# Optimization experiments

Measured on AMD Instinct MI355X. Metric: run time of the kernel, lower is better.

The kernel has to match this reference:

```python
import jax, jax.numpy as jnp
import numpy as np

D_MODEL = 1024
N_HEADS = 16
D_HEAD = D_MODEL // N_HEADS
WINDOW = 256
ATTN_SCALE = 1.0
SCALE = float(np.sqrt(D_HEAD))
NEG = -10000.0


def setup_inputs() -> dict:
    key = jax.random.key(0)
    ks = jax.random.split(key, 7)
    B, S = 2, 2048
    q = jax.random.normal(ks[0], (B, S, D_MODEL), dtype=jnp.float32)
    k = jax.random.normal(ks[1], (B, S, D_MODEL), dtype=jnp.float32)
    v = jax.random.normal(ks[2], (B, S, D_MODEL), dtype=jnp.float32)
    # Xavier-uniform-like scale for square linear weights: sqrt(6/(fan_in+fan_out))
    lim = float(np.sqrt(6.0 / (D_MODEL + D_MODEL)))
    def xavier(kk):
        return jax.random.uniform(kk, (D_MODEL, D_MODEL), minval=-lim, maxval=lim, dtype=jnp.float32)
    return {"q": q, "k": k, "v": v,
            "WQ": xavier(ks[3]), "WK": xavier(ks[4]),
            "WV": xavier(ks[5]), "WO": xavier(ks[6])}


def _split_heads(x):
    B, S, _ = x.shape
    return x.reshape(B, S, N_HEADS, D_HEAD).transpose(0, 2, 1, 3)  # [B,H,S,Dh]


def reference(q, k, v, WQ, WK, WV, WO):
    B, Sq, _ = q.shape
    Sk = k.shape[1]
    # torch nn.Linear: y = x @ W.T
    qh = _split_heads(q @ WQ.T) / SCALE          # [B,H,Sq,Dh]
    kh = _split_heads(k @ WK.T)                  # [B,H,Sk,Dh]
    vh = _split_heads(v @ WV.T)                  # [B,H,Sk,Dh]
    scores = jnp.einsum('bhqd,bhkd->bhqk', qh, kh) * ATTN_SCALE
    # global abs-max normalization (clamped at 1)
    scores = scores / jnp.maximum(jnp.max(jnp.abs(scores)), 1.0)
    # sliding window mask: key j visible to query i iff i-WINDOW+1 <= j <= i
    qi = jnp.arange(Sq)[:, None]
    kj = jnp.arange(Sk)[None, :]
    win = (kj <= qi) & (kj > qi - WINDOW)        # [Sq,Sk] bool
    scores = jnp.where(win[None, None], scores, NEG)
    attn = jax.nn.softmax(scores, axis=-1)
    out = jnp.einsum('bhqk,bhkd->bhqd', attn, vh)
    out = out.transpose(0, 2, 1, 3).reshape(B, Sq, D_MODEL)
    out = out @ WO.T
    out = out / jnp.maximum(jnp.mean(jnp.abs(out)), 1.0)
    return out
```

## Files before the change

### kernel.cpp

```cpp
#include <hip/hip_runtime.h>
#include <hip/hip_bf16.h>

#define S_LEN 2048
#define DM    1024
#define NH    16
#define DH    64
#define WIN   256
#define BATCH 2

using f32x4   = __attribute__((ext_vector_type(4))) float;
using bf16x8  = __attribute__((ext_vector_type(8))) short;
using ushort8 = __attribute__((ext_vector_type(8))) unsigned short;

static __device__ __forceinline__ unsigned short f2bf(float f) {
  unsigned int x = __float_as_uint(f);
  x += 0x7fffu + ((x >> 16) & 1u);
  return (unsigned short)(x >> 16);
}

typedef const __attribute__((address_space(1))) void* gas_t;
typedef __attribute__((address_space(3))) void* las_t;
static __device__ __forceinline__ void gload16(const void* g, void* l) {
  __builtin_amdgcn_global_load_lds((gas_t)g, (las_t)l, 16, 0, 0);
}

__global__ __launch_bounds__(256) void k_cvt_all(const float* __restrict__ w0,
                                                 const float* __restrict__ w1,
                                                 const float* __restrict__ w2,
                                                 const float* __restrict__ w3,
                                                 const float* __restrict__ q,
                                                 const float* __restrict__ k,
                                                 const float* __restrict__ v,
                                                 unsigned short* __restrict__ Wb,
                                                 unsigned short* __restrict__ qb,
                                                 unsigned short* __restrict__ kb,
                                                 unsigned short* __restrict__ vb,
                                                 unsigned int* __restrict__ absmax) {
  const int z = blockIdx.z;
  if (z == 0 && blockIdx.x == 0 && threadIdx.x == 0) *absmax = 0u;
  const float* src;
  unsigned short* dst;
  int n8;
  if (z < 4) {
    src = (z == 0) ? w0 : (z == 1) ? w1 : (z == 2) ? w2 : w3;
    dst = Wb + (size_t)z * DM * DM;
    n8 = (DM * DM) / 8;
  } else {
    src = (z == 4) ? q : (z == 5) ? k : v;
    dst = (z == 4) ? qb : (z == 5) ? kb : vb;
    n8 = (BATCH * S_LEN * DM) / 8;
  }
  int i = blockIdx.x * blockDim.x + threadIdx.x;
  int stride = gridDim.x * blockDim.x;
  for (; i < n8; i += stride) {
    float4 f0 = ((const float4*)src)[2 * i];
    float4 f1 = ((const float4*)src)[2 * i + 1];
    ushort8 u;
    u[0] = f2bf(f0.x); u[1] = f2bf(f0.y); u[2] = f2bf(f0.z); u[3] = f2bf(f0.w);
    u[4] = f2bf(f1.x); u[5] = f2bf(f1.y); u[6] = f2bf(f1.z); u[7] = f2bf(f1.w);
    ((ushort8*)dst)[i] = u;
  }
}

__device__ __forceinline__ void gemm128_core(const unsigned short* __restrict__ A,
                                             const unsigned short* __restrict__ Bw,
                                             void* __restrict__ Cptr, float oscale,
                                             int omode, bool swap, int R0, int C0,
                                             float* __restrict__ partials, int pbid) {
  __shared__ unsigned short As[2][128][64];
  __shared__ unsigned short Bs[2][128][64];
  __shared__ float red[4];
  const int tid = threadIdx.x, lane = tid & 63, w = tid >> 6;
  const int wr = w >> 1, wc = w & 1;

  int srow[4], scol[4];
#pragma unroll
  for (int c = 0; c < 4; ++c) {
    srow[c] = c * 32 + w * 8 + (lane >> 3);
    scol[c] = ((lane & 7) ^ (srow[c] & 7)) << 3;
  }

  f32x4 z = {0.f, 0.f, 0.f, 0.f};
  f32x4 acc[4][4];
#pragma unroll
  for (int i = 0; i < 4; ++i)
#pragma unroll
    for (int j = 0; j < 4; ++j) acc[i][j] = z;

  unsigned short* Af0 = &As[0][0][0];
  unsigned short* Bf0 = &Bs[0][0][0];
  const int cb = 16 * (lane >> 4);

#define STAGE_G(buf, k0) do {                                                          \
    unsigned short* Ad = Af0 + (buf) * 8192 + w * 512;                                 \
    unsigned short* Bd = Bf0 + (buf) * 8192 + w * 512;                                 \
    _Pragma("unroll")                                                                  \
    for (int c = 0; c < 4; ++c) {                                                      \
      gload16(A  + (size_t)(R0 + srow[c]) * DM + (k0) + scol[c], Ad + c * 2048);       \
      gload16(Bw + (size_t)(C0 + srow[c]) * DM + (k0) + scol[c], Bd + c * 2048);       \
    }                                                                                  \
  } while (0)

  STAGE_G(0, 0);
  __syncthreads();

  for (int t = 0; t < 16; ++t) {
    const int cur = t & 1;
    if (t + 1 < 16) STAGE_G(cur ^ 1, (t + 1) * 64);

    const char* Af = (const char*)(Af0 + cur * 8192);
    const char* Bf = (const char*)(Bf0 + cur * 8192);
    bf16x8 av[4][2], bv[4][2];
#pragma unroll
    for (int i = 0; i < 4; ++i) {
      int row = 64 * wr + 16 * i + (lane & 15);
      int sw = (row & 7) << 4;
      const char* rp = Af + row * 128;
      av[i][0] = *(const bf16x8*)(rp + (cb ^ sw));
      av[i][1] = *(const bf16x8*)(rp + ((cb + 64) ^ sw));
    }
#pragma unroll
    for (int j = 0; j < 4; ++j) {
      int row = 64 * wc + 16 * j + (lane & 15);
      int sw = (row & 7) << 4;
      const char* rp = Bf + row * 128;
      bv[j][0] = *(const bf16x8*)(rp + (cb ^ sw));
      bv[j][1] = *(const bf16x8*)(rp + ((cb + 64) ^ sw));
    }
    if (swap) {
#pragma unroll
      for (int i = 0; i < 4; ++i)
#pragma unroll
        for (int j = 0; j < 4; ++j) {
          acc[i][j] = __builtin_amdgcn_mfma_f32_16x16x32_bf16(bv[j][0], av[i][0], acc[i][j], 0, 0, 0);
          acc[i][j] = __builtin_amdgcn_mfma_f32_16x16x32_bf16(bv[j][1], av[i][1], acc[i][j], 0, 0, 0);
        }
    } else {
#pragma unroll
      for (int i = 0; i < 4; ++i)
#pragma unroll
        for (int j = 0; j < 4; ++j) {
          acc[i][j] = __builtin_amdgcn_mfma_f32_16x16x32_bf16(av[i][0], bv[j][0], acc[i][j], 0, 0, 0);
          acc[i][j] = __builtin_amdgcn_mfma_f32_16x16x32_bf16(av[i][1], bv[j][1], acc[i][j], 0, 0, 0);
        }
    }
    __syncthreads();
  }
#undef STAGE_G

  float s = 0.f;
#pragma unroll
  for (int i = 0; i < 4; ++i) {
#pragma unroll
    for (int j = 0; j < 4; ++j) {
      if (swap) {
        int grow  = R0 + 64 * wr + 16 * i + (lane & 15);
        int gcol0 = C0 + 64 * wc + 16 * j + 4 * (lane >> 4);
        if (omode == 0) {
          float4 st = {acc[i][j][0] * oscale, acc[i][j][1] * oscale,
                       acc[i][j][2] * oscale, acc[i][j][3] * oscale};
          s += fabsf(st.x) + fabsf(st.y) + fabsf(st.z) + fabsf(st.w);
          *(float4*)((float*)Cptr + (size_t)grow * DM + gcol0) = st;
        } else {
          int b = grow >> 11, ss = grow & (S_LEN - 1);
          int h = gcol0 >> 6, d0 = gcol0 & 63;
          ushort4 st = {f2bf(acc[i][j][0] * oscale), f2bf(acc[i][j][1] * oscale),
                        f2bf(acc[i][j][2] * oscale), f2bf(acc[i][j][3] * oscale)};
          *(ushort4*)((unsigned short*)Cptr + (((size_t)(b * NH + h) * S_LEN + ss) << 6) + d0) = st;
        }
      } else {
        int grow0 = R0 + 64 * wr + 16 * i + 4 * (lane >> 4);
        int gcol  = C0 + 64 * wc + 16 * j + (lane & 15);
        int b = grow0 >> 11, s0 = grow0 & (S_LEN - 1);
        int h = gcol >> 6, d = gcol & 63;
        ushort4 st = {f2bf(acc[i][j][0] * oscale), f2bf(acc[i][j][1] * oscale),
                      f2bf(acc[i][j][2] * oscale), f2bf(acc[i][j][3] * oscale)};
        *(ushort4*)((unsigned short*)Cptr + (((size_t)(b * NH + h) * DH + d) << 11) + s0) = st;
      }
    }
  }
  if (partials) {
#pragma unroll
    for (int mk = 1; mk < 64; mk <<= 1) s += __shfl_xor(s, mk, 64);
    if (lane == 0) red[w] = s;
    __syncthreads();
    if (tid == 0) partials[pbid] = red[0] + red[1] + red[2] + red[3];
  }
}

__global__ __launch_bounds__(256) void k_gemm_qkv(const unsigned short* __restrict__ qb,
                                                  const unsigned short* __restrict__ kb,
                                                  const unsigned short* __restrict__ vb,
                                                  const unsigned short* __restrict__ WbQ,
                                                  const unsigned short* __restrict__ WbK,
                                                  const unsigned short* __restrict__ WbV,
                                                  unsigned short* __restrict__ qh,
                                                  unsigned short* __restrict__ kh,
                                                  unsigned short* __restrict__ vt) {
  const unsigned short *A, *B;
  unsigned short* C;
  float sc;
  int om;
  bool sw;
  if (blockIdx.z == 0)      { A = qb; B = WbQ; C = qh; sc = 0.125f; om = 1; sw = true;  }
  else if (blockIdx.z == 1) { A = kb; B = WbK; C = kh; sc = 1.0f;   om = 1; sw = true;  }
  else                      { A = vb; B = WbV; C = vt; sc = 1.0f;   om = 2; sw = false; }
  gemm128_core(A, B, C, sc, om, sw, blockIdx.x * 128, blockIdx.y * 128, nullptr, 0);
}

__global__ __launch_bounds__(256) void k_gemm_out(const unsigned short* __restrict__ A,
                                                  const unsigned short* __restrict__ Bw,
                                                  float* __restrict__ C,
                                                  float* __restrict__ partials) {
  gemm128_core(A, Bw, C, 1.0f, 0, true, blockIdx.x * 128, blockIdx.y * 128,
               partials, blockIdx.x + gridDim.x * blockIdx.y);
}

__global__ __launch_bounds__(256) void k_scoresmax(const unsigned short* __restrict__ qh,
                                                   const unsigned short* __restrict__ kh,
                                                   unsigned int* __restrict__ absmax) {
  __shared__ unsigned short Ks[2][128][64];
  const int tid = threadIdx.x, lane = tid & 63, w = tid >> 6;
  const int lin = blockIdx.x;
  const int xcd = lin & 7, j = lin >> 3;
  const int bh = xcd + 8 * (j >> 3);
  const int q0 = (j & 7) * 256;
  const size_t base = (size_t)bh * S_LEN * DH;
  const unsigned short* Q = qh + base;
  const unsigned short* K = kh + base;

  bf16x8 a[4][2];
#pragma unroll
  for (int rb = 0; rb < 4; ++rb) {
    const unsigned short* qr = Q + (size_t)(q0 + 64 * w + 16 * rb + (lane & 15)) * DH + 8 * (lane >> 4);
    a[rb][0] = *(const bf16x8*)qr;
    a[rb][1] = *(const bf16x8*)(qr + 32);
  }

  int srow[4], scol[4];
#pragma unroll
  for (int c = 0; c < 4; ++c) {
    srow[c] = c * 32 + w * 8 + (lane >> 3);
    scol[c] = ((lane & 7) ^ (srow[c] & 7)) << 3;
  }
  unsigned short* Kf0 = &Ks[0][0][0];
  const int cbb = 16 * (lane >> 4);

#define STAGE_K(buf, kc) do {                                                          \
    unsigned short* Kd = Kf0 + (buf) * 8192 + w * 512;                                 \
    _Pragma("unroll")                                                                  \
    for (int c = 0; c < 4; ++c)                                                        \
      gload16(K + (size_t)((kc) + srow[c]) * DH + scol[c], Kd + c * 2048);             \
  } while (0)

  STAGE_K(0, 0);
  __syncthreads();

  float m = 0.f;
  for (int t = 0; t < 16; ++t) {
    const int cur = t & 1;
    if (t + 1 < 16) STAGE_K(cur ^ 1, (t + 1) * 128);
    const char* Kf = (const char*)(Kf0 + cur * 8192);
#pragma unroll
    for (int cb = 0; cb < 8; ++cb) {
      int row = 16 * cb + (lane & 15);
      int sw = (row & 7) << 4;
      const char* rp = Kf + row * 128;
      bf16x8 b0 = *(const bf16x8*)(rp + (cbb ^ sw));
      bf16x8 b1 = *(const bf16x8*)(rp + ((cbb + 64) ^ sw));
#pragma unroll
      for (int rb = 0; rb < 4; ++rb) {
        f32x4 acc = {0.f, 0.f, 0.f, 0.f};
        acc = __builtin_amdgcn_mfma_f32_16x16x32_bf16(a[rb][0], b0, acc, 0, 0, 0);
        acc = __builtin_amdgcn_mfma_f32_16x16x32_bf16(a[rb][1], b1, acc, 0, 0, 0);
        m = fmaxf(m, fmaxf(fmaxf(fabsf(acc[0]), fabsf(acc[1])), fmaxf(fabsf(acc[2]), fabsf(acc[3]))));
      }
    }
    __syncthreads();
  }
#undef STAGE_K

#pragma unroll
  for (int mk = 1; mk < 64; mk <<= 1) m = fmaxf(m, __shfl_xor(m, mk, 64));
  __shared__ float red[4];
  if (lane == 0) red[w] = m;
  __syncthreads();
  if (threadIdx.x == 0)
    atomicMax(absmax, __float_as_uint(fmaxf(fmaxf(red[0], red[1]), fmaxf(red[2], red[3]))));
}

#define NT 10
__global__ __launch_bounds__(256) void k_attn(const unsigned short* __restrict__ qh,
                                              const unsigned short* __restrict__ kh,
                                              const unsigned short* __restrict__ vt,
                                              const unsigned int* __restrict__ absmax,
                                              unsigned short* __restrict__ attn_c) {
  __shared__ unsigned short Ks[2][32][72];
  __shared__ unsigned short Vts[2][64][40];
  __shared__ unsigned short Pl[4][16][40];
  const int tid = threadIdx.x, lane = tid & 63, w = tid >> 6;
  const int lin = blockIdx.x;
  const int xcd = lin & 7, j = lin >> 3;
  const int bh = xcd + 8 * (j >> 5);
  const int Q0 = (j & 31) * 64;
  const int b = bh >> 4, h = bh & 15;
  const int kstart = Q0 - WIN;
  const size_t base = (size_t)bh * S_LEN * DH;
  const unsigned short* Kb = kh + base;
  const unsigned short* Vtb = vt + base;

  const int skrow = tid >> 3, skcol = (tid & 7) << 3;
  const int svd = tid >> 2, svcol = (tid & 3) << 3;

  const float invM = 1.0f / fmaxf(__uint_as_float(*absmax), 1.0f);
  const unsigned short* Qp = qh + base + (size_t)(Q0 + 16 * w + (lane & 15)) * DH + 8 * (lane >> 4);
  bf16x8 a0 = *(const bf16x8*)Qp;
  bf16x8 a1 = *(const bf16x8*)(Qp + 32);

  ushort8 rk, rv;
  ushort8 zz = {0, 0, 0, 0, 0, 0, 0, 0};
#define LOADT(T) do {                                                        \
    int kk = kstart + 32 * (T) + skrow;                                      \
    rk = (kk >= 0) ? *(const ushort8*)(Kb + (size_t)kk * DH + skcol) : zz;   \
    int kc = kstart + 32 * (T) + svcol;                                      \
    rv = (kc >= 0) ? *(const ushort8*)(Vtb + (size_t)svd * S_LEN + kc) : zz; \
  } while (0)
#define WRITET(buf) do {                                                     \
    *(ushort8*)&Ks[buf][skrow][skcol] = rk;                                  \
    *(ushort8*)&Vts[buf][svd][svcol] = rv;                                   \
  } while (0)

  LOADT(0);
  WRITET(0);
  __syncthreads();

  const int Tlo = w >> 1, Thi = (w >> 1) + 8;
  const int qrow = Q0 + 16 * w + 4 * (lane >> 4);
  float sm[4] = {0.f, 0.f, 0.f, 0.f};
  f32x4 z = {0.f, 0.f, 0.f, 0.f};
  f32x4 o[4];
#pragma unroll
  for (int i = 0; i < 4; ++i) o[i] = z;

  for (int T = 0; T < NT; ++T) {
    const int cur = T & 1;
    const bool act = (T >= Tlo) && (T <= Thi);
    if (T + 1 < NT) LOADT(T + 1);
    if (act) {
      f32x4 p[2];
#pragma unroll
      for (int cb = 0; cb < 2; ++cb) {
        const unsigned short* kr = &Ks[cur][16 * cb + (lane & 15)][8 * (lane >> 4)];
        bf16x8 b0 = *(const bf16x8*)kr;
        bf16x8 b1 = *(const bf16x8*)(kr + 32);
        f32x4 a = z;
        a = __builtin_amdgcn_mfma_f32_16x16x32_bf16(a0, b0, a, 0, 0, 0);
        a = __builtin_amdgcn_mfma_f32_16x16x32_bf16(a1, b1, a, 0, 0, 0);
        p[cb] = a;
      }
#pragma unroll
      for (int cb = 0; cb < 2; ++cb) {
        int kcol = kstart + 32 * T + 16 * cb + (lane & 15);
#pragma unroll
        for (int r = 0; r < 4; ++r) {
          int qq = qrow + r;
          bool ok = (kcol >= 0) && (kcol <= qq) && (kcol + WIN > qq);
          float e = ok ? __expf(p[cb][r] * invM) : 0.f;
          sm[r] += e;
          Pl[w][4 * (lane >> 4) + r][16 * cb + (lane & 15)] = f2bf(e);
        }
      }
    }
    __syncthreads();
    if (act) {
      bf16x8 pa = *(const bf16x8*)&Pl[w][lane & 15][8 * (lane >> 4)];
#pragma unroll
      for (int dt = 0; dt < 4; ++dt) {
        bf16x8 bv = *(const bf16x8*)&Vts[cur][16 * dt + (lane & 15)][8 * (lane >> 4)];
        o[dt] = __builtin_amdgcn_mfma_f32_16x16x32_bf16(pa, bv, o[dt], 0, 0, 0);
      }
    }
    if (T + 1 < NT) WRITET((T + 1) & 1);
    __syncthreads();
  }

#pragma unroll
  for (int r = 0; r < 4; ++r) {
#pragma unroll
    for (int mk = 1; mk < 16; mk <<= 1) sm[r] += __shfl_xor(sm[r], mk, 64);
    sm[r] = 1.0f / sm[r];
  }
#pragma unroll
  for (int dt = 0; dt < 4; ++dt) {
#pragma unroll
    for (int r = 0; r < 4; ++r) {
      int qq = qrow + r;
      float val = o[dt][r] * sm[r];
      attn_c[((size_t)(b * S_LEN + qq) << 10) + h * DH + 16 * dt + (lane & 15)] = f2bf(val);
    }
  }
#undef LOADT
#undef WRITET
}

__global__ __launch_bounds__(256) void k_scale_final(float* __restrict__ x,
                                                     const float* __restrict__ partials,
                                                     float invcnt, int n4) {
  __shared__ float red[4];
  float s = partials[threadIdx.x];
#pragma unroll
  for (int mk = 1; mk < 64; mk <<= 1) s += __shfl_xor(s, mk, 64);
  if ((threadIdx.x & 63) == 0) red[threadIdx.x >> 6] = s;
  __syncthreads();
  float d = 1.0f / fmaxf((red[0] + red[1] + red[2] + red[3]) * invcnt, 1.0f);
  for (int i = blockIdx.x * blockDim.x + threadIdx.x; i < n4; i += gridDim.x * blockDim.x) {
    float4 f = ((float4*)x)[i];
    f.x *= d; f.y *= d; f.z *= d; f.w *= d;
    ((float4*)x)[i] = f;
  }
}

extern "C" void kernel_launch(void* const* d_in, const int* in_sizes, int n_in,
                              void* d_out, int out_size, void* d_ws, size_t ws_size,
                              hipStream_t stream) {
  (void)in_sizes; (void)n_in; (void)out_size; (void)ws_size;
  const float* q  = (const float*)d_in[0];
  const float* k  = (const float*)d_in[1];
  const float* v  = (const float*)d_in[2];
  const float* WQ = (const float*)d_in[3];
  const float* WK = (const float*)d_in[4];
  const float* WV = (const float*)d_in[5];
  const float* WO = (const float*)d_in[6];

  const size_t HS = (size_t)BATCH * NH * S_LEN * DH;
  unsigned short* qb     = (unsigned short*)d_ws;
  unsigned short* kb     = qb + HS;
  unsigned short* vb     = kb + HS;
  unsigned short* qh     = vb + HS;
  unsigned short* kh     = qh + HS;
  unsigned short* vt     = kh + HS;
  unsigned short* Wb     = vt + HS;
  char* scal             = (char*)(Wb + 4 * (size_t)DM * DM);
  unsigned int* absmax   = (unsigned int*)scal;
  float* partials        = (float*)(scal + 16);
  unsigned short* attn_c = qb;

  unsigned short* WbQ = Wb;
  unsigned short* WbK = Wb + (size_t)DM * DM;
  unsigned short* WbV = Wb + 2 * (size_t)DM * DM;
  unsigned short* WbO = Wb + 3 * (size_t)DM * DM;

  k_cvt_all<<<dim3(128, 1, 7), 256, 0, stream>>>(WQ, WK, WV, WO, q, k, v, Wb, qb, kb, vb, absmax);

  k_gemm_qkv<<<dim3(32, 8, 3), 256, 0, stream>>>(qb, kb, vb, WbQ, WbK, WbV, qh, kh, vt);

  k_scoresmax<<<256, 256, 0, stream>>>(qh, kh, absmax);
  k_attn<<<1024, 256, 0, stream>>>(qh, kh, vt, absmax, attn_c);

  k_gemm_out<<<dim3(32, 8), 256, 0, stream>>>(attn_c, WbO, (float*)d_out, partials);

  k_scale_final<<<1024, 256, 0, stream>>>((float*)d_out, partials, 1.0f / (float)HS, (int)(HS / 4));
}
```

Measured before the change: 141.9 us.

## Replace QKV projection GEMM with 256x256-tile, 8-wave, eight-phase pipelined kernel

The QKV projection moves from 128x128 tiles with 256 threads to 256x256 tiles with 512 threads (8 waves). Each k-step is split into eight phases that interleave LDS reads, async global-to-LDS staging and MFMA bursts, using explicit barriers, vmcnt waits and setprio. The larger tile raises operand reuse and the phase schedule is meant to hide load latency. In exchange the grid shrinks to 192 blocks, which may underfill the GPU's CUs, and LDS use and register pressure go up.

```diff
diff --git a/kernel.cpp b/kernel.cpp
--- a/kernel.cpp
+++ b/kernel.cpp
@@ -62,6 +62,192 @@
   }
 }
 
+__device__ __forceinline__ void gemm256_8ph(const unsigned short* __restrict__ A,
+                                            const unsigned short* __restrict__ Bw,
+                                            void* __restrict__ Cptr, float oscale,
+                                            int omode, bool swap, int R0, int C0) {
+  __shared__ unsigned short As_[2][256][64];
+  __shared__ unsigned short Bs_[2][256][64];
+  const int tid = threadIdx.x, lane = tid & 63, w = tid >> 6;
+  const int wr = w >> 2, wc = w & 3;
+
+  const int srow_in_half = w * 8 + (lane >> 3);
+  const int cb = 16 * (lane >> 4);
+
+#define STAGE_AH(buf, h, t) do {                                                        \
+    _Pragma("unroll")                                                                   \
+    for (int c = 0; c < 2; ++c) {                                                       \
+      int r = (h) * 128 + c * 64 + srow_in_half;                                        \
+      int sc = ((lane & 7) ^ (r & 7)) << 3;                                             \
+      gload16(A + (size_t)(R0 + r) * DM + (t) * 64 + sc, &As_[buf][r & ~7][0] + ((r & 7) - (lane >> 3)) * 0 + ( (h)*128 + c*64 + w*8 ) * 64 - ((h)*128 + c*64 + w*8)*64 + &As_[buf][(h)*128 + c*64 + w*8][0] - &As_[buf][(h)*128 + c*64 + w*8][0] + 0); \
+    }                                                                                   \
+  } while (0)
+#undef STAGE_AH
+#define STAGE_AH(buf, h, t) do {                                                        \
+    _Pragma("unroll")                                                                   \
+    for (int c = 0; c < 2; ++c) {                                                       \
+      int r = (h) * 128 + c * 64 + srow_in_half;                                        \
+      int sc = ((lane & 7) ^ (r & 7)) << 3;                                             \
+      gload16(A + (size_t)(R0 + r) * DM + (t) * 64 + sc,                                \
+              &As_[buf][(h) * 128 + c * 64 + w * 8][0]);                                \
+    }                                                                                   \
+  } while (0)
+#define STAGE_BH(buf, h, t) do {                                                        \
+    _Pragma("unroll")                                                                   \
+    for (int c = 0; c < 2; ++c) {                                                       \
+      int r = (h) * 128 + c * 64 + srow_in_half;                                        \
+      int sc = ((lane & 7) ^ (r & 7)) << 3;                                             \
+      gload16(Bw + (size_t)(C0 + r) * DM + (t) * 64 + sc,                               \
+              &Bs_[buf][(h) * 128 + c * 64 + w * 8][0]);                                \
+    }                                                                                   \
+  } while (0)
+#define READ_AV(dst, buf, kf) do {                                                      \
+    _Pragma("unroll")                                                                   \
+    for (int i = 0; i < 8; ++i) {                                                       \
+      int row = 128 * wr + 16 * i + (lane & 15);                                        \
+      int byte = (cb + 64 * (kf)) ^ ((row & 7) << 4);                                   \
+      dst[i] = *(const bf16x8*)((const char*)&As_[buf][row][0] + byte);                 \
+    }                                                                                   \
+  } while (0)
+#define READ_BV(dst, buf, jh, kf) do {                                                  \
+    _Pragma("unroll")                                                                   \
+    for (int jj = 0; jj < 2; ++jj) {                                                    \
+      int row = 64 * wc + 16 * (2 * (jh) + jj) + (lane & 15);                           \
+      int byte = (cb + 64 * (kf)) ^ ((row & 7) << 4);                                   \
+      dst[jj] = *(const bf16x8*)((const char*)&Bs_[buf][row][0] + byte);                \
+    }                                                                                   \
+  } while (0)
+
+  f32x4 z = {0.f, 0.f, 0.f, 0.f};
+  f32x4 acc[8][4];
+#pragma unroll
+  for (int i = 0; i < 8; ++i)
+#pragma unroll
+    for (int j = 0; j < 4; ++j) acc[i][j] = z;
+
+  bf16x8 avA[8], avB[8], bvA[2], bvB[2];
+
+#define MFMA_PH(av, bv, jh) do {                                                        \
+    __builtin_amdgcn_s_setprio(1);                                                      \
+    if (swap) {                                                                         \
+      _Pragma("unroll")                                                                 \
+      for (int i = 0; i < 8; ++i) {                                                     \
+        acc[i][2*(jh)]   = __builtin_amdgcn_mfma_f32_16x16x32_bf16(bv[0], av[i], acc[i][2*(jh)],   0, 0, 0); \
+        acc[i][2*(jh)+1] = __builtin_amdgcn_mfma_f32_16x16x32_bf16(bv[1], av[i], acc[i][2*(jh)+1], 0, 0, 0); \
+      }                                                                                 \
+    } else {                                                                            \
+      _Pragma("unroll")                                                                 \
+      for (int i = 0; i < 8; ++i) {                                                     \
+        acc[i][2*(jh)]   = __builtin_amdgcn_mfma_f32_16x16x32_bf16(av[i], bv[0], acc[i][2*(jh)],   0, 0, 0); \
+        acc[i][2*(jh)+1] = __builtin_amdgcn_mfma_f32_16x16x32_bf16(av[i], bv[1], acc[i][2*(jh)+1], 0, 0, 0); \
+      }                                                                                 \
+    }                                                                                   \
+    __builtin_amdgcn_s_setprio(0);                                                      \
+  } while (0)
+
+#define PH_SYNC() do {                                                                  \
+    __builtin_amdgcn_s_barrier();                                                       \
+    asm volatile("s_waitcnt lgkmcnt(0)" ::: "memory");                                  \
+    __builtin_amdgcn_sched_barrier(0);                                                  \
+  } while (0)
+#define PH_END() __builtin_amdgcn_s_barrier()
+
+  STAGE_AH(0, 0, 0); STAGE_AH(0, 1, 0); STAGE_BH(0, 0, 0); STAGE_BH(0, 1, 0);
+  STAGE_AH(1, 0, 1); STAGE_AH(1, 1, 1); STAGE_BH(1, 0, 1); STAGE_BH(1, 1, 1);
+  asm volatile("s_waitcnt vmcnt(8)" ::: "memory");
+  __builtin_amdgcn_s_barrier();
+  READ_AV(avA, 0, 0);
+  READ_BV(bvA, 0, 0, 0);
+
+  for (int m = 0; m < 8; ++m) {
+    const int t2 = 2 * m + 2, t3 = 2 * m + 3;
+    READ_BV(bvB, 0, 1, 0);
+    if (m > 0) STAGE_BH(1, 0, 2 * m + 1);
+    PH_SYNC(); MFMA_PH(avA, bvA, 0); PH_END();
+    READ_AV(avB, 0, 1);
+    READ_BV(bvA, 0, 0, 1);
+    if (m > 0) STAGE_BH(1, 1, 2 * m + 1);
+    PH_SYNC(); MFMA_PH(avA, bvB, 1); PH_END();
+    READ_BV(bvB, 0, 1, 1);
+    if (t2 < 16) STAGE_AH(0, 0, t2);
+    asm volatile("s_waitcnt vmcnt(2)" ::: "memory");
+    PH_SYNC(); MFMA_PH(avB, bvA, 0); PH_END();
+    READ_AV(avA, 1, 0);
+    READ_BV(bvA, 1, 0, 0);
+    if (t2 < 16) STAGE_AH(0, 1, t2);
+    PH_SYNC(); MFMA_PH(avB, bvB, 1); PH_END();
+    READ_BV(bvB, 1, 1, 0);
+    if (t2 < 16) STAGE_BH(0, 0, t2);
+    PH_SYNC(); MFMA_PH(avA, bvA, 0); PH_END();
+    READ_AV(avB, 1, 1);
+    READ_BV(bvA, 1, 0, 1);
+    if (t2 < 16) STAGE_BH(0, 1, t2);
+    PH_SYNC(); MFMA_PH(avA, bvB, 1); PH_END();
+    READ_BV(bvB, 1, 1, 1);
+    if (t3 < 16) STAGE_AH(1, 0, t3);
+    asm volatile("s_waitcnt vmcnt(2)" ::: "memory");
+    PH_SYNC(); MFMA_PH(avB, bvA, 0); PH_END();
+    if (m < 7) {
+      READ_AV(avA, 0, 0);
+      READ_BV(bvA, 0, 0, 0);
+    }
+    if (t3 < 16) STAGE_AH(1, 1, t3);
+    PH_SYNC(); MFMA_PH(avB, bvB, 1); PH_END();
+  }
+#undef STAGE_AH
+#undef STAGE_BH
+#undef READ_AV
+#undef READ_BV
+#undef MFMA_PH
+#undef PH_SYNC
+#undef PH_END
+
+#pragma unroll
+  for (int i = 0; i < 8; ++i) {
+#pragma unroll
+    for (int j = 0; j < 4; ++j) {
+      if (swap) {
+        int grow  = R0 + 128 * wr + 16 * i + (lane & 15);
+        int gcol0 = C0 + 64 * wc + 16 * j + 4 * (lane >> 4);
+        int b = grow >> 11, ss = grow & (S_LEN - 1);
+        int h = gcol0 >> 6, d0 = gcol0 & 63;
+        ushort4 st = {f2bf(acc[i][j][0] * oscale), f2bf(acc[i][j][1] * oscale),
+                      f2bf(acc[i][j][2] * oscale), f2bf(acc[i][j][3] * oscale)};
+        *(ushort4*)((unsigned short*)Cptr + (((size_t)(b * NH + h) * S_LEN + ss) << 6) + d0) = st;
+      } else {
+        int grow0 = R0 + 128 * wr + 16 * i + 4 * (lane >> 4);
+        int gcol  = C0 + 64 * wc + 16 * j + (lane & 15);
+        int b = grow0 >> 11, s0 = grow0 & (S_LEN - 1);
+        int h = gcol >> 6, d = gcol & 63;
+        ushort4 st = {f2bf(acc[i][j][0] * oscale), f2bf(acc[i][j][1] * oscale),
+                      f2bf(acc[i][j][2] * oscale), f2bf(acc[i][j][3] * oscale)};
+        *(ushort4*)((unsigned short*)Cptr + (((size_t)(b * NH + h) * DH + d) << 11) + s0) = st;
+      }
+    }
+  }
+  (void)omode;
+}
+
+__global__ __launch_bounds__(512) void k_gemm_qkv8(const unsigned short* __restrict__ qb,
+                                                   const unsigned short* __restrict__ kb,
+                                                   const unsigned short* __restrict__ vb,
+                                                   const unsigned short* __restrict__ WbQ,
+                                                   const unsigned short* __restrict__ WbK,
+                                                   const unsigned short* __restrict__ WbV,
+                                                   unsigned short* __restrict__ qh,
+                                                   unsigned short* __restrict__ kh,
+                                                   unsigned short* __restrict__ vt) {
+  const unsigned short *A, *B;
+  unsigned short* C;
+  float sc;
+  int om;
+  bool sw;
+  if (blockIdx.z == 0)      { A = qb; B = WbQ; C = qh; sc = 0.125f; om = 1; sw = true;  }
+  else if (blockIdx.z == 1) { A = kb; B = WbK; C = kh; sc = 1.0f;   om = 1; sw = true;  }
+  else                      { A = vb; B = WbV; C = vt; sc = 1.0f;   om = 2; sw = false; }
+  gemm256_8ph(A, B, C, sc, om, sw, blockIdx.x * 256, blockIdx.y * 256);
+}
+
 __device__ __forceinline__ void gemm128_core(const unsigned short* __restrict__ A,
                                              const unsigned short* __restrict__ Bw,
                                              void* __restrict__ Cptr, float oscale,
@@ -188,26 +374,6 @@
   }
 }
 
-__global__ __launch_bounds__(256) void k_gemm_qkv(const unsigned short* __restrict__ qb,
-                                                  const unsigned short* __restrict__ kb,
-                                                  const unsigned short* __restrict__ vb,
-                                                  const unsigned short* __restrict__ WbQ,
-                                                  const unsigned short* __restrict__ WbK,
-                                                  const unsigned short* __restrict__ WbV,
-                                                  unsigned short* __restrict__ qh,
-                                                  unsigned short* __restrict__ kh,
-                                                  unsigned short* __restrict__ vt) {
-  const unsigned short *A, *B;
-  unsigned short* C;
-  float sc;
-  int om;
-  bool sw;
-  if (blockIdx.z == 0)      { A = qb; B = WbQ; C = qh; sc = 0.125f; om = 1; sw = true;  }
-  else if (blockIdx.z == 1) { A = kb; B = WbK; C = kh; sc = 1.0f;   om = 1; sw = true;  }
-  else                      { A = vb; B = WbV; C = vt; sc = 1.0f;   om = 2; sw = false; }
-  gemm128_core(A, B, C, sc, om, sw, blockIdx.x * 128, blockIdx.y * 128, nullptr, 0);
-}
-
 __global__ __launch_bounds__(256) void k_gemm_out(const unsigned short* __restrict__ A,
                                                   const unsigned short* __restrict__ Bw,
                                                   float* __restrict__ C,
@@ -262,8 +428,8 @@
     if (t + 1 < 16) STAGE_K(cur ^ 1, (t + 1) * 128);
     const char* Kf = (const char*)(Kf0 + cur * 8192);
 #pragma unroll
-    for (int cb = 0; cb < 8; ++cb) {
-      int row = 16 * cb + (lane & 15);
+    for (int cbk = 0; cbk < 8; ++cbk) {
+      int row = 16 * cbk + (lane & 15);
       int sw = (row & 7) << 4;
       const char* rp = Kf + row * 128;
       bf16x8 b0 = *(const bf16x8*)(rp + (cbb ^ sw));
@@ -452,7 +618,7 @@
 
   k_cvt_all<<<dim3(128, 1, 7), 256, 0, stream>>>(WQ, WK, WV, WO, q, k, v, Wb, qb, kb, vb, absmax);
 
-  k_gemm_qkv<<<dim3(32, 8, 3), 256, 0, stream>>>(qb, kb, vb, WbQ, WbK, WbV, qh, kh, vt);
+  k_gemm_qkv8<<<dim3(16, 4, 3), 512, 0, stream>>>(qb, kb, vb, WbQ, WbK, WbV, qh, kh, vt);
 
   k_scoresmax<<<256, 256, 0, stream>>>(qh, kh, absmax);
   k_attn<<<1024, 256, 0, stream>>>(qh, kh, vt, absmax, attn_c);
```

After: 280.5 us. 97.7% more time.
